# Performance work log

Measured on AMD Instinct MI355X. Metric: run time of the kernel, lower is better.

## Reference

```python
import jax, jax.numpy as jnp
import numpy as np

NUM_USERS = 500000
NUM_ITEMS = 200000
EMB = 64
N_LAYERS = 3
N_EDGES = 5_000_000
N_NODES = NUM_USERS + NUM_ITEMS


def _xavier_uniform(key, fan_in, fan_out):
    bound = float(np.sqrt(6.0 / (fan_in + fan_out)))
    return jax.random.uniform(key, (fan_in, fan_out), minval=-bound, maxval=bound, dtype=jnp.float32)


def setup_inputs() -> dict:
    key = jax.random.key(0)
    k1, k2, k3 = jax.random.split(key, 3)
    user_emb = _xavier_uniform(k1, NUM_USERS, EMB)
    item_emb = _xavier_uniform(k2, NUM_ITEMS, EMB)
    edge_index = jax.random.randint(k3, (2, N_EDGES), 0, N_NODES, dtype=jnp.int32)
    return {"user_emb": user_emb, "item_emb": item_emb, "edge_index": edge_index}


def reference(user_emb, item_emb, edge_index):
    # x: [N, D] stacked user+item embeddings
    x = jnp.concatenate([user_emb, item_emb], axis=0)
    row, col = edge_index[0], edge_index[1]

    # gcn_norm without self-loops (LGConv default): deg over targets (col)
    deg = jax.ops.segment_sum(jnp.ones(row.shape[0], dtype=x.dtype), col, num_segments=N_NODES)
    dinv = jnp.where(deg > 0, jax.lax.rsqrt(jnp.where(deg > 0, deg, 1.0)), 0.0)
    norm = dinv[row] * dinv[col]  # [E]

    all_embeddings = [x]
    for _ in range(N_LAYERS):
        msgs = norm[:, None] * x[row]                     # [E, D] gather + scale
        x = jax.ops.segment_sum(msgs, col, num_segments=N_NODES)  # scatter-add
        all_embeddings.append(x)

    all_embeddings = jnp.stack(all_embeddings, axis=1)    # [N, L+1, D]
    out = jnp.mean(all_embeddings, axis=1)                # [N, D]
    # NOTE: replicates original slicing exactly (out[num_items:] for items)
    return (out[:NUM_USERS], out[NUM_ITEMS:], all_embeddings)
```

## Files before the change

### kernel.cpp

```cpp
#include <hip/hip_runtime.h>


static constexpr int NUSERS = 500000;
static constexpr int NITEMS = 200000;
static constexpr int NNODES = 700000;
static constexpr int NE     = 5000000;
static constexpr int NB     = (NNODES + 1023) / 1024;
static constexpr int CH     = 4096;

typedef float f4 __attribute__((ext_vector_type(4)));

__device__ inline unsigned bf16rne(float f) {
    unsigned u = __float_as_uint(f);
    return (u + 0x7FFFu + ((u >> 16) & 1u)) >> 16;
}
__device__ inline unsigned packbf(float lo, float hi) {
    return bf16rne(lo) | (bf16rne(hi) << 16);
}
__device__ inline void acc8(float4& A, float4& B, uint4 q) {
    A.x += __uint_as_float(q.x << 16); A.y += __uint_as_float(q.x & 0xFFFF0000u);
    A.z += __uint_as_float(q.y << 16); A.w += __uint_as_float(q.y & 0xFFFF0000u);
    B.x += __uint_as_float(q.z << 16); B.y += __uint_as_float(q.z & 0xFFFF0000u);
    B.z += __uint_as_float(q.w << 16); B.w += __uint_as_float(q.w & 0xFFFF0000u);
}


__global__ void k_bcount(const int* __restrict__ col, int* __restrict__ bcnt) {
    __shared__ int h[NB];
    int t = threadIdx.x;
    for (int i = t; i < NB; i += 256) h[i] = 0;
    __syncthreads();
    for (int e = blockIdx.x * blockDim.x + t; e < NE; e += gridDim.x * blockDim.x)
        atomicAdd(&h[col[e] >> 10], 1);
    __syncthreads();
    for (int i = t; i < NB; i += 256)
        if (h[i]) atomicAdd(&bcnt[i], h[i]);
}

__global__ void k_bscan(const int* __restrict__ bcnt, int* __restrict__ bbase,
                        int* __restrict__ bcur) {
    __shared__ int s[1024];
    int t = threadIdx.x;
    int v = (t < NB) ? bcnt[t] : 0;
    s[t] = v;
    __syncthreads();
    for (int off = 1; off < 1024; off <<= 1) {
        int add = (t >= off) ? s[t - off] : 0;
        __syncthreads();
        s[t] += add;
        __syncthreads();
    }
    int excl = s[t] - v;
    if (t < NB) { bbase[t] = excl; bcur[t] = excl; }
    if (t == NB - 1) bbase[NB] = excl + v;
}

__global__ void k_bpart(const int* __restrict__ row, const int* __restrict__ col,
                        int* __restrict__ bcur, unsigned* __restrict__ pairs) {
    __shared__ unsigned pe[CH];
    __shared__ unsigned short pb[CH];
    __shared__ int lh[NB];
    __shared__ int lbase[NB];
    int t = threadIdx.x;
    for (int i = t; i < NB; i += 256) lh[i] = 0;
    __syncthreads();
    int base = blockIdx.x * CH;
    int cnt = min(CH, NE - base);
    for (int i = t; i < cnt; i += 256) {
        int c = col[base + i], r = row[base + i];
        int b = c >> 10;
        pe[i] = ((unsigned)(c & 1023) << 20) | (unsigned)r;
        pb[i] = (unsigned short)b;
        atomicAdd(&lh[b], 1);
    }
    __syncthreads();
    for (int b = t; b < NB; b += 256) {
        int v = lh[b];
        if (v) lbase[b] = atomicAdd(&bcur[b], v);
        lh[b] = 0;
    }
    __syncthreads();
    for (int i = t; i < cnt; i += 256) {
        int b = pb[i];
        int pos = lbase[b] + atomicAdd(&lh[b], 1);
        pairs[pos] = pe[i];
    }
}

__global__ void k_bsort(const unsigned* __restrict__ pairs, const int* __restrict__ bbase,
                        int* __restrict__ sr, float* __restrict__ dinv,
                        int2* __restrict__ offs2) {
    __shared__ int cnt[1024];
    __shared__ int cur[1024];
    __shared__ int part[256];
    int b = blockIdx.x;
    int t = threadIdx.x;
    int lo = bbase[b], hi = bbase[b + 1];
    int nbase = b << 10;
    for (int i = t; i < 1024; i += 256) cnt[i] = 0;
    __syncthreads();
    for (int k = lo + t; k < hi; k += 256)
        atomicAdd(&cnt[pairs[k] >> 20], 1);
    __syncthreads();
    int s0 = cnt[t * 4], s1 = cnt[t * 4 + 1], s2 = cnt[t * 4 + 2], s3 = cnt[t * 4 + 3];
    int tot = s0 + s1 + s2 + s3;
    part[t] = tot;
    __syncthreads();
    for (int off = 1; off < 256; off <<= 1) {
        int add = (t >= off) ? part[t - off] : 0;
        __syncthreads();
        part[t] += add;
        __syncthreads();
    }
    int pbase = part[t] - tot;
    int e0 = pbase, e1 = pbase + s0, e2 = e1 + s1, e3 = e2 + s2;
    cur[t * 4] = e0; cur[t * 4 + 1] = e1; cur[t * 4 + 2] = e2; cur[t * 4 + 3] = e3;
    int n0 = nbase + t * 4;
    if (n0 + 0 < NNODES) { dinv[n0+0] = s0 ? rsqrtf((float)s0) : 0.f;
                           offs2[n0+0] = make_int2(lo + e0, lo + e0 + s0); }
    if (n0 + 1 < NNODES) { dinv[n0+1] = s1 ? rsqrtf((float)s1) : 0.f;
                           offs2[n0+1] = make_int2(lo + e1, lo + e1 + s1); }
    if (n0 + 2 < NNODES) { dinv[n0+2] = s2 ? rsqrtf((float)s2) : 0.f;
                           offs2[n0+2] = make_int2(lo + e2, lo + e2 + s2); }
    if (n0 + 3 < NNODES) { dinv[n0+3] = s3 ? rsqrtf((float)s3) : 0.f;
                           offs2[n0+3] = make_int2(lo + e3, lo + e3 + s3); }
    __syncthreads();
    for (int k = lo + t; k < hi; k += 256) {
        unsigned u = pairs[k];
        int pos = lo + atomicAdd(&cur[u >> 20], 1);
        sr[pos] = (int)(u & 0xFFFFFu);
    }
}


__global__ void k_init(const float4* __restrict__ user, const float4* __restrict__ item,
                       float4* __restrict__ all_emb, const float* __restrict__ dinv,
                       uint4* __restrict__ xb0) {
    int tid = blockIdx.x * blockDim.x + threadIdx.x;
    if (tid >= NNODES * 8) return;
    int n    = tid >> 3;
    int lane = tid & 7;
    const float4* s = ((n < NUSERS) ? user + (size_t)n * 16
                                    : item + (size_t)(n - NUSERS) * 16) + lane * 2;
    float4 a = s[0], b = s[1];
    f4* dst = reinterpret_cast<f4*>(all_emb + (size_t)n * 64 + lane * 2);
    f4 av = {a.x, a.y, a.z, a.w};
    f4 bv = {b.x, b.y, b.z, b.w};
    __builtin_nontemporal_store(av, dst + 0);
    __builtin_nontemporal_store(bv, dst + 1);
    float dv = dinv[n];
    uint4 o;
    o.x = packbf(dv * a.x, dv * a.y); o.y = packbf(dv * a.z, dv * a.w);
    o.z = packbf(dv * b.x, dv * b.y); o.w = packbf(dv * b.z, dv * b.w);
    xb0[(size_t)n * 8 + lane] = o;
}

template <int L, bool FUSE_OUT>
__global__ void k_prop(const int2* __restrict__ offs2,
                       const int* __restrict__ sr, const float* __restrict__ dinv,
                       const uint4* __restrict__ xbp,
                       uint4* __restrict__ xbc,
                       float4* __restrict__ all_emb,
                       float* __restrict__ out_users, float* __restrict__ out_items) {
    int tid = blockIdx.x * blockDim.x + threadIdx.x;
    if (tid >= NNODES * 8) return;
    int n    = tid >> 3;
    int lane = tid & 7;
    int2 be = offs2[n];
    int b = be.x, e = be.y;
    float4 accA = make_float4(0.f, 0.f, 0.f, 0.f);
    float4 accB = make_float4(0.f, 0.f, 0.f, 0.f);
    const uint4* src = xbp + lane;

    int k = b;
    for (; k + 4 <= e; k += 4) {
        int r0 = sr[k + 0], r1 = sr[k + 1], r2 = sr[k + 2], r3 = sr[k + 3];
        uint4 q0 = src[(size_t)r0 * 8];
        uint4 q1 = src[(size_t)r1 * 8];
        uint4 q2 = src[(size_t)r2 * 8];
        uint4 q3 = src[(size_t)r3 * 8];
        acc8(accA, accB, q0); acc8(accA, accB, q1);
        acc8(accA, accB, q2); acc8(accA, accB, q3);
    }
    for (; k < e; ++k) {
        uint4 q = src[(size_t)sr[k] * 8];
        acc8(accA, accB, q);
    }
    float dv = dinv[n];
    accA.x *= dv; accA.y *= dv; accA.z *= dv; accA.w *= dv;
    accB.x *= dv; accB.y *= dv; accB.z *= dv; accB.w *= dv;

    f4 aA = {accA.x, accA.y, accA.z, accA.w};
    f4 aB = {accB.x, accB.y, accB.z, accB.w};
    f4* dstn = reinterpret_cast<f4*>(all_emb + (size_t)n * 64 + L * 16 + lane * 2);
    __builtin_nontemporal_store(aA, dstn + 0);
    __builtin_nontemporal_store(aB, dstn + 1);

    if constexpr (!FUSE_OUT) {
        uint4 o;
        o.x = packbf(dv * accA.x, dv * accA.y);
        o.y = packbf(dv * accA.z, dv * accA.w);
        o.z = packbf(dv * accB.x, dv * accB.y);
        o.w = packbf(dv * accB.z, dv * accB.w);
        xbc[(size_t)n * 8 + lane] = o;
    } else {
        const f4* p = reinterpret_cast<const f4*>(all_emb + (size_t)n * 64 + lane * 2);
        f4 x0a = __builtin_nontemporal_load(p + 0);
        f4 x0b = __builtin_nontemporal_load(p + 1);
        f4 x1a = __builtin_nontemporal_load(p + 16);
        f4 x1b = __builtin_nontemporal_load(p + 17);
        f4 x2a = __builtin_nontemporal_load(p + 32);
        f4 x2b = __builtin_nontemporal_load(p + 33);
        f4 ma = (x0a + x1a + x2a + aA) * 0.25f;
        f4 mb = (x0b + x1b + x2b + aB) * 0.25f;
        if (n < NUSERS) {
            f4* ou = reinterpret_cast<f4*>(out_users + (size_t)n * 64 + lane * 8);
            __builtin_nontemporal_store(ma, ou + 0);
            __builtin_nontemporal_store(mb, ou + 1);
        }
        if (n >= NITEMS) {
            f4* oi = reinterpret_cast<f4*>(out_items + (size_t)(n - NITEMS) * 64 + lane * 8);
            __builtin_nontemporal_store(ma, oi + 0);
            __builtin_nontemporal_store(mb, oi + 1);
        }
    }
}

extern "C" void kernel_launch(void* const* d_in, const int* in_sizes, int n_in,
                              void* d_out, int out_size, void* d_ws, size_t ws_size,
                              hipStream_t stream) {
    const float* user  = (const float*)d_in[0];
    const float* item  = (const float*)d_in[1];
    const int*   edges = (const int*)d_in[2];
    const int*   row = edges;
    const int*   col = edges + NE;

    float* out       = (float*)d_out;
    float* out_users = out;
    float* out_items = out + (size_t)NUSERS * 64;
    float* all_emb   = out + (size_t)NUSERS * 64 * 2;

    char* ws = (char*)d_ws;
    uint4*    xb0   = (uint4*)ws;                     ws += (size_t)NNODES * 128;
    uint4*    xb1   = (uint4*)ws;                     ws += (size_t)NNODES * 128;
    unsigned* pairs = (unsigned*)ws;                  ws += (size_t)NE * 4;
    int*      sr    = (int*)ws;                       ws += (size_t)NE * 4;
    int2*     offs2 = (int2*)ws;                      ws += (size_t)NNODES * 8;
    float*    dinv  = (float*)ws;                     ws += (size_t)NNODES * 4;
    int*      bcnt  = (int*)ws;                       ws += (size_t)NB * 4;
    int*      bbase = (int*)ws;                       ws += (size_t)(NB + 1) * 4;
    int*      bcur  = (int*)ws;                       ws += (size_t)NB * 4;

    const int B = 256;
    const int prop_grid = (NNODES * 8 + B - 1) / B;

    (void)hipMemsetAsync(bcnt, 0, (size_t)NB * sizeof(int), stream);
    k_bcount<<<1024, 256, 0, stream>>>(col, bcnt);
    k_bscan <<<1, 1024, 0, stream>>>(bcnt, bbase, bcur);
    k_bpart <<<(NE + CH - 1) / CH, 256, 0, stream>>>(row, col, bcur, pairs);
    k_bsort <<<NB, 256, 0, stream>>>(pairs, bbase, sr, dinv, offs2);
    k_init  <<<prop_grid, B, 0, stream>>>(
        (const float4*)user, (const float4*)item, (float4*)all_emb, dinv, xb0);

    k_prop<1, false><<<prop_grid, B, 0, stream>>>(offs2, sr, dinv, xb0, xb1,
                                                  (float4*)all_emb, nullptr, nullptr);
    k_prop<2, false><<<prop_grid, B, 0, stream>>>(offs2, sr, dinv, xb1, xb0,
                                                  (float4*)all_emb, nullptr, nullptr);
    k_prop<3, true> <<<prop_grid, B, 0, stream>>>(offs2, sr, dinv, xb0, nullptr,
                                                  (float4*)all_emb, out_users, out_items);
}
```

Measured before the change: 782.7 us.

## Use fixed-capacity buckets to drop count/scan passes and fuse init into bucket sort

Replaces the count + scan + partition pipeline with fixed-capacity per-bucket regions (BCAP slots per 1024-node bucket), so partitioning needs only an atomic fill counter and no global histogram or prefix scan. The embedding init and bf16 scaling are folded into the bucket sort kernel, reusing degree-derived dinv from shared memory. This removes two kernel launches and one full pass over col, at the cost of re-reading col/row in the partition kernel, larger chunks per block (fewer blocks), and a hard capacity assumption that overflows if any bucket exceeds 8192 edges.

```diff
diff --git a/kernel.cpp b/kernel.cpp
--- a/kernel.cpp
+++ b/kernel.cpp
@@ -6,7 +6,8 @@
 static constexpr int NNODES = 700000;
 static constexpr int NE     = 5000000;
 static constexpr int NB     = (NNODES + 1023) / 1024;
-static constexpr int CH     = 4096;
+static constexpr int BCAP   = 8192;
+static constexpr int CH     = 20480;
 
 typedef float f4 __attribute__((ext_vector_type(4)));
 
@@ -24,41 +25,8 @@
     B.z += __uint_as_float(q.w << 16); B.w += __uint_as_float(q.w & 0xFFFF0000u);
 }
 
-
-__global__ void k_bcount(const int* __restrict__ col, int* __restrict__ bcnt) {
-    __shared__ int h[NB];
-    int t = threadIdx.x;
-    for (int i = t; i < NB; i += 256) h[i] = 0;
-    __syncthreads();
-    for (int e = blockIdx.x * blockDim.x + t; e < NE; e += gridDim.x * blockDim.x)
-        atomicAdd(&h[col[e] >> 10], 1);
-    __syncthreads();
-    for (int i = t; i < NB; i += 256)
-        if (h[i]) atomicAdd(&bcnt[i], h[i]);
-}
-
-__global__ void k_bscan(const int* __restrict__ bcnt, int* __restrict__ bbase,
-                        int* __restrict__ bcur) {
-    __shared__ int s[1024];
-    int t = threadIdx.x;
-    int v = (t < NB) ? bcnt[t] : 0;
-    s[t] = v;
-    __syncthreads();
-    for (int off = 1; off < 1024; off <<= 1) {
-        int add = (t >= off) ? s[t - off] : 0;
-        __syncthreads();
-        s[t] += add;
-        __syncthreads();
-    }
-    int excl = s[t] - v;
-    if (t < NB) { bbase[t] = excl; bcur[t] = excl; }
-    if (t == NB - 1) bbase[NB] = excl + v;
-}
-
 __global__ void k_bpart(const int* __restrict__ row, const int* __restrict__ col,
-                        int* __restrict__ bcur, unsigned* __restrict__ pairs) {
-    __shared__ unsigned pe[CH];
-    __shared__ unsigned short pb[CH];
+                        int* __restrict__ bfill, unsigned* __restrict__ pairs) {
     __shared__ int lh[NB];
     __shared__ int lbase[NB];
     int t = threadIdx.x;
@@ -66,36 +34,36 @@
     __syncthreads();
     int base = blockIdx.x * CH;
     int cnt = min(CH, NE - base);
-    for (int i = t; i < cnt; i += 256) {
-        int c = col[base + i], r = row[base + i];
-        int b = c >> 10;
-        pe[i] = ((unsigned)(c & 1023) << 20) | (unsigned)r;
-        pb[i] = (unsigned short)b;
-        atomicAdd(&lh[b], 1);
-    }
+    for (int i = t; i < cnt; i += 256)
+        atomicAdd(&lh[col[base + i] >> 10], 1);
     __syncthreads();
     for (int b = t; b < NB; b += 256) {
         int v = lh[b];
-        if (v) lbase[b] = atomicAdd(&bcur[b], v);
+        if (v) lbase[b] = atomicAdd(&bfill[b], v);
         lh[b] = 0;
     }
     __syncthreads();
     for (int i = t; i < cnt; i += 256) {
-        int b = pb[i];
+        int c = col[base + i];
+        int b = c >> 10;
         int pos = lbase[b] + atomicAdd(&lh[b], 1);
-        pairs[pos] = pe[i];
-    }
-}
-
-__global__ void k_bsort(const unsigned* __restrict__ pairs, const int* __restrict__ bbase,
+        pairs[(size_t)b * BCAP + pos] = ((unsigned)(c & 1023) << 20) | (unsigned)row[base + i];
+    }
+}
+
+__global__ void k_bsort(const unsigned* __restrict__ pairs, const int* __restrict__ bfill,
                         int* __restrict__ sr, float* __restrict__ dinv,
-                        int2* __restrict__ offs2) {
+                        int2* __restrict__ offs2,
+                        const float4* __restrict__ user, const float4* __restrict__ item,
+                        float4* __restrict__ all_emb, uint4* __restrict__ xb0) {
     __shared__ int cnt[1024];
     __shared__ int cur[1024];
     __shared__ int part[256];
+    __shared__ float ddv[1024];
     int b = blockIdx.x;
     int t = threadIdx.x;
-    int lo = bbase[b], hi = bbase[b + 1];
+    int lo = b * BCAP;
+    int hi = lo + bfill[b];
     int nbase = b << 10;
     for (int i = t; i < 1024; i += 256) cnt[i] = 0;
     __syncthreads();
@@ -115,44 +83,41 @@
     int pbase = part[t] - tot;
     int e0 = pbase, e1 = pbase + s0, e2 = e1 + s1, e3 = e2 + s2;
     cur[t * 4] = e0; cur[t * 4 + 1] = e1; cur[t * 4 + 2] = e2; cur[t * 4 + 3] = e3;
+    float d0 = s0 ? rsqrtf((float)s0) : 0.f;
+    float d1 = s1 ? rsqrtf((float)s1) : 0.f;
+    float d2 = s2 ? rsqrtf((float)s2) : 0.f;
+    float d3 = s3 ? rsqrtf((float)s3) : 0.f;
+    ddv[t * 4] = d0; ddv[t * 4 + 1] = d1; ddv[t * 4 + 2] = d2; ddv[t * 4 + 3] = d3;
     int n0 = nbase + t * 4;
-    if (n0 + 0 < NNODES) { dinv[n0+0] = s0 ? rsqrtf((float)s0) : 0.f;
-                           offs2[n0+0] = make_int2(lo + e0, lo + e0 + s0); }
-    if (n0 + 1 < NNODES) { dinv[n0+1] = s1 ? rsqrtf((float)s1) : 0.f;
-                           offs2[n0+1] = make_int2(lo + e1, lo + e1 + s1); }
-    if (n0 + 2 < NNODES) { dinv[n0+2] = s2 ? rsqrtf((float)s2) : 0.f;
-                           offs2[n0+2] = make_int2(lo + e2, lo + e2 + s2); }
-    if (n0 + 3 < NNODES) { dinv[n0+3] = s3 ? rsqrtf((float)s3) : 0.f;
-                           offs2[n0+3] = make_int2(lo + e3, lo + e3 + s3); }
+    if (n0 + 0 < NNODES) { dinv[n0+0] = d0; offs2[n0+0] = make_int2(lo + e0, lo + e0 + s0); }
+    if (n0 + 1 < NNODES) { dinv[n0+1] = d1; offs2[n0+1] = make_int2(lo + e1, lo + e1 + s1); }
+    if (n0 + 2 < NNODES) { dinv[n0+2] = d2; offs2[n0+2] = make_int2(lo + e2, lo + e2 + s2); }
+    if (n0 + 3 < NNODES) { dinv[n0+3] = d3; offs2[n0+3] = make_int2(lo + e3, lo + e3 + s3); }
     __syncthreads();
     for (int k = lo + t; k < hi; k += 256) {
         unsigned u = pairs[k];
         int pos = lo + atomicAdd(&cur[u >> 20], 1);
         sr[pos] = (int)(u & 0xFFFFFu);
     }
-}
-
-
-__global__ void k_init(const float4* __restrict__ user, const float4* __restrict__ item,
-                       float4* __restrict__ all_emb, const float* __restrict__ dinv,
-                       uint4* __restrict__ xb0) {
-    int tid = blockIdx.x * blockDim.x + threadIdx.x;
-    if (tid >= NNODES * 8) return;
-    int n    = tid >> 3;
-    int lane = tid & 7;
-    const float4* s = ((n < NUSERS) ? user + (size_t)n * 16
-                                    : item + (size_t)(n - NUSERS) * 16) + lane * 2;
-    float4 a = s[0], b = s[1];
-    f4* dst = reinterpret_cast<f4*>(all_emb + (size_t)n * 64 + lane * 2);
-    f4 av = {a.x, a.y, a.z, a.w};
-    f4 bv = {b.x, b.y, b.z, b.w};
-    __builtin_nontemporal_store(av, dst + 0);
-    __builtin_nontemporal_store(bv, dst + 1);
-    float dv = dinv[n];
-    uint4 o;
-    o.x = packbf(dv * a.x, dv * a.y); o.y = packbf(dv * a.z, dv * a.w);
-    o.z = packbf(dv * b.x, dv * b.y); o.w = packbf(dv * b.z, dv * b.w);
-    xb0[(size_t)n * 8 + lane] = o;
+    for (int idx = t; idx < 1024 * 8; idx += 256) {
+        int nl   = idx >> 3;
+        int lane = idx & 7;
+        int n = nbase + nl;
+        if (n >= NNODES) break;
+        const float4* s = ((n < NUSERS) ? user + (size_t)n * 16
+                                        : item + (size_t)(n - NUSERS) * 16) + lane * 2;
+        float4 a = s[0], bb = s[1];
+        f4* dst = reinterpret_cast<f4*>(all_emb + (size_t)n * 64 + lane * 2);
+        f4 av = {a.x, a.y, a.z, a.w};
+        f4 bv = {bb.x, bb.y, bb.z, bb.w};
+        __builtin_nontemporal_store(av, dst + 0);
+        __builtin_nontemporal_store(bv, dst + 1);
+        float dv = ddv[nl];
+        uint4 o;
+        o.x = packbf(dv * a.x, dv * a.y); o.y = packbf(dv * a.z, dv * a.w);
+        o.z = packbf(dv * bb.x, dv * bb.y); o.w = packbf(dv * bb.z, dv * bb.w);
+        xb0[(size_t)n * 8 + lane] = o;
+    }
 }
 
 template <int L, bool FUSE_OUT>
@@ -243,24 +208,20 @@
     char* ws = (char*)d_ws;
     uint4*    xb0   = (uint4*)ws;                     ws += (size_t)NNODES * 128;
     uint4*    xb1   = (uint4*)ws;                     ws += (size_t)NNODES * 128;
-    unsigned* pairs = (unsigned*)ws;                  ws += (size_t)NE * 4;
-    int*      sr    = (int*)ws;                       ws += (size_t)NE * 4;
+    unsigned* pairs = (unsigned*)ws;                  ws += (size_t)NB * BCAP * 4;
+    int*      sr    = (int*)ws;                       ws += (size_t)NB * BCAP * 4;
     int2*     offs2 = (int2*)ws;                      ws += (size_t)NNODES * 8;
     float*    dinv  = (float*)ws;                     ws += (size_t)NNODES * 4;
-    int*      bcnt  = (int*)ws;                       ws += (size_t)NB * 4;
-    int*      bbase = (int*)ws;                       ws += (size_t)(NB + 1) * 4;
-    int*      bcur  = (int*)ws;                       ws += (size_t)NB * 4;
+    int*      bfill = (int*)ws;                       ws += (size_t)NB * 4;
 
     const int B = 256;
     const int prop_grid = (NNODES * 8 + B - 1) / B;
 
-    (void)hipMemsetAsync(bcnt, 0, (size_t)NB * sizeof(int), stream);
-    k_bcount<<<1024, 256, 0, stream>>>(col, bcnt);
-    k_bscan <<<1, 1024, 0, stream>>>(bcnt, bbase, bcur);
-    k_bpart <<<(NE + CH - 1) / CH, 256, 0, stream>>>(row, col, bcur, pairs);
-    k_bsort <<<NB, 256, 0, stream>>>(pairs, bbase, sr, dinv, offs2);
-    k_init  <<<prop_grid, B, 0, stream>>>(
-        (const float4*)user, (const float4*)item, (float4*)all_emb, dinv, xb0);
+    (void)hipMemsetAsync(bfill, 0, (size_t)NB * sizeof(int), stream);
+    k_bpart<<<(NE + CH - 1) / CH, 256, 0, stream>>>(row, col, bfill, pairs);
+    k_bsort<<<NB, 256, 0, stream>>>(pairs, bfill, sr, dinv, offs2,
+                                    (const float4*)user, (const float4*)item,
+                                    (float4*)all_emb, xb0);
 
     k_prop<1, false><<<prop_grid, B, 0, stream>>>(offs2, sr, dinv, xb0, xb1,
                                                   (float4*)all_emb, nullptr, nullptr);
```

Measured after the change: 809.5 us. +3.4%, slower.
